# Kernel tuning notes

Hardware: AMD Instinct MI355X
Metric: run time of the kernel (lower is better)

## Reference

```python
import jax, jax.numpy as jnp
import numpy as np

N_AB, N_AG, F = 20000, 20000, 256
E_AB, E_AG, E_D = 320000, 320000, 640000
EPS = 1e-5


def _bn(x, gamma, beta):
    # BatchNorm1d, training-mode batch statistics (deterministic), biased variance
    mu = x.mean(0)
    var = x.var(0)
    return (x - mu) * jax.lax.rsqrt(var + EPS) * gamma + beta


def _gcn(x, ei, W, b, n):
    # PyG GCNConv: add self loops, symmetric deg^-1/2 normalization, scatter-add
    loop = jnp.arange(n, dtype=ei.dtype)
    src = jnp.concatenate([ei[0], loop])
    dst = jnp.concatenate([ei[1], loop])
    deg = jax.ops.segment_sum(jnp.ones_like(src, dtype=x.dtype), dst, num_segments=n)
    dinv = jax.lax.rsqrt(jnp.maximum(deg, 1.0))  # deg >= 1 due to self loops
    norm = dinv[src] * dinv[dst]                 # [E]
    h = x @ W                                    # [n, D]
    return jax.ops.segment_sum(h[src] * norm[:, None], dst, num_segments=n) + b


def _gat(x, ei, W, a_s, a_d, b, n, slope=0.2):
    # PyG GATConv, heads=1, add self loops; attention dropout off (eval mode)
    loop = jnp.arange(n, dtype=ei.dtype)
    src = jnp.concatenate([ei[0], loop])
    dst = jnp.concatenate([ei[1], loop])
    h = x @ W                                    # [n, D]
    e = jax.nn.leaky_relu((h @ a_s)[src] + (h @ a_d)[dst], slope)  # [E]
    # segment softmax over incoming edges of each dst node
    m = jax.ops.segment_max(e, dst, num_segments=n)
    ex = jnp.exp(e - m[dst])
    s = jax.ops.segment_sum(ex, dst, num_segments=n)
    alpha = ex / s[dst]
    return jax.ops.segment_sum(h[src] * alpha[:, None], dst, num_segments=n) + b


def setup_inputs() -> dict:
    key = jax.random.key(0)
    ks = jax.random.split(key, 20)
    sc = 1.0 / np.sqrt(F)
    sc2 = 1.0 / np.sqrt(2 * F)
    inp = {
        "x_ab": jax.random.normal(ks[0], (N_AB, F), jnp.float32),
        "x_ag": jax.random.normal(ks[1], (N_AG, F), jnp.float32),
        "W_gcn": jax.random.normal(ks[2], (F, F), jnp.float32) * sc,
        "b_gcn": jnp.zeros((F,), jnp.float32),
        "g1": jnp.ones((F,), jnp.float32),
        "be1": jnp.zeros((F,), jnp.float32),
        "W_aggcn": jax.random.normal(ks[3], (F, F), jnp.float32) * sc,
        "b_aggcn": jnp.zeros((F,), jnp.float32),
        "ag_g1": jnp.ones((F,), jnp.float32),
        "ag_be1": jnp.zeros((F,), jnp.float32),
        "W_gat": jax.random.normal(ks[4], (F, F), jnp.float32) * sc,
        "a_src": jax.random.normal(ks[5], (F,), jnp.float32) * sc,
        "a_dst": jax.random.normal(ks[6], (F,), jnp.float32) * sc,
        "b_gat": jnp.zeros((F,), jnp.float32),
        "W_gat2": jax.random.normal(ks[7], (F, F), jnp.float32) * sc,
        "a_src2": jax.random.normal(ks[8], (F,), jnp.float32) * sc,
        "a_dst2": jax.random.normal(ks[9], (F,), jnp.float32) * sc,
        "b_gat2": jnp.zeros((F,), jnp.float32),
        "ag_g2": jnp.ones((2 * F,), jnp.float32),
        "ag_be2": jnp.zeros((2 * F,), jnp.float32),
        "W_agfc": jax.random.normal(ks[10], (2 * F, 1), jnp.float32) * sc2,
        "b_agfc": jnp.zeros((1,), jnp.float32),
        "g2": jnp.ones((2 * F,), jnp.float32),
        "be2": jnp.zeros((2 * F,), jnp.float32),
        "W_fc": jax.random.normal(ks[11], (2 * F, 1), jnp.float32) * sc2,
        "b_fc": jnp.zeros((1,), jnp.float32),
        "edge_x_ab": jax.random.randint(ks[12], (2, E_AB), 0, N_AB, jnp.int32),
        "edge_x_ag": jax.random.randint(ks[13], (2, E_AG), 0, N_AG, jnp.int32),
        "edge_index_d": jax.random.randint(ks[14], (2, E_D), 0, N_AB + N_AG, jnp.int32),
    }
    return inp


def reference(x_ab, x_ag, W_gcn, b_gcn, g1, be1, W_aggcn, b_aggcn, ag_g1, ag_be1,
              W_gat, a_src, a_dst, b_gat, W_gat2, a_src2, a_dst2, b_gat2,
              ag_g2, ag_be2, W_agfc, b_agfc, g2, be2, W_fc, b_fc,
              edge_x_ab, edge_x_ag, edge_index_d):
    relu = jax.nn.relu
    h_ab = relu(_bn(_gcn(x_ab, edge_x_ab, W_gcn, b_gcn, N_AB), g1, be1))
    h_ag = relu(_bn(_gcn(x_ag, edge_x_ag, W_aggcn, b_aggcn, N_AG), ag_g1, ag_be1))
    # dropout layers are identity in eval mode
    n = N_AB + N_AG
    x = jnp.concatenate([h_ab, h_ag], axis=0)
    x = relu(_gat(x, edge_index_d, W_gat, a_src, a_dst, b_gat, n))
    x = _gat(x, edge_index_d, W_gat2, a_src2, a_dst2, b_gat2, n)
    x1, x2 = x[:N_AB], x[N_AB:]
    out_ag = relu(_bn(jnp.concatenate([x2, h_ag], axis=1), ag_g2, ag_be2)) @ W_agfc + b_agfc
    out_ab = relu(_bn(jnp.concatenate([x1, h_ab], axis=1), g2, be2)) @ W_fc + b_fc
    return out_ab, out_ag
```

## Files before the change

kernel.cpp:

```cpp
#include <hip/hip_runtime.h>
#include <hip/hip_bf16.h>
#include <stdint.h>

#define NF 256
#define EPSV 1e-5f
#define PB 160
#define MAXBUK 160

typedef unsigned short u16;
typedef unsigned int u32;
typedef short short8 __attribute__((ext_vector_type(8)));
typedef float floatx4 __attribute__((ext_vector_type(4)));

#define P_BGCN 0
#define P_G1 256
#define P_BE1 512
#define P_BAGG 768
#define P_AGG1 1024
#define P_AGBE1 1280
#define P_ASRC 1536
#define P_ADST 1792
#define P_BGAT 2048
#define P_ASRC2 2304
#define P_ADST2 2560
#define P_BGAT2 2816
#define P_G2 3072
#define P_BE2 3584
#define P_WFC 4096
#define P_AGG2 4608
#define P_AGBE2 5120
#define P_WAGFC 5632
#define P_BFC 6144
#define P_BAGFC 6145

__device__ __forceinline__ float bf2f(u16 u) {
    union { unsigned int i; float f; } v; v.i = ((unsigned int)u) << 16; return v.f;
}
__device__ __forceinline__ u16 f2bf(float f) {
    unsigned int x = __float_as_uint(f);
    unsigned int r = x + 0x7fffu + ((x >> 16) & 1u);
    return (u16)(r >> 16);
}
__device__ __forceinline__ float sane(float f) {
    return (f == f && fabsf(f) < 1e30f) ? f : 0.f;
}
__device__ __forceinline__ unsigned int zap2(unsigned int w) {
    if ((w & 0x00007F80u) == 0x00007F80u) w &= 0xFFFF0000u;
    if ((w & 0x7F800000u) == 0x7F800000u) w &= 0x0000FFFFu;
    return w;
}
__device__ __forceinline__ float lrelu(float x) { return x > 0.f ? x : 0.2f * x; }

__device__ __forceinline__ float4 ld4h(const u16* p) {
    uint2 u = *(const uint2*)p;
    float4 r;
    r.x = bf2f((u16)(u.x & 0xFFFFu)); r.y = bf2f((u16)(u.x >> 16));
    r.z = bf2f((u16)(u.y & 0xFFFFu)); r.w = bf2f((u16)(u.y >> 16));
    return r;
}
__device__ __forceinline__ void st4h(u16* p, float4 v) {
    uint2 u;
    u.x = (unsigned)f2bf(v.x) | ((unsigned)f2bf(v.y) << 16);
    u.y = (unsigned)f2bf(v.z) | ((unsigned)f2bf(v.w) << 16);
    *(uint2*)p = u;
}

__device__ __forceinline__ void fma8(const uint4 u, float a, float* acc) {
    acc[0] = fmaf(__uint_as_float(u.x << 16), a, acc[0]);
    acc[1] = fmaf(__uint_as_float(u.x & 0xFFFF0000u), a, acc[1]);
    acc[2] = fmaf(__uint_as_float(u.y << 16), a, acc[2]);
    acc[3] = fmaf(__uint_as_float(u.y & 0xFFFF0000u), a, acc[3]);
    acc[4] = fmaf(__uint_as_float(u.z << 16), a, acc[4]);
    acc[5] = fmaf(__uint_as_float(u.z & 0xFFFF0000u), a, acc[5]);
    acc[6] = fmaf(__uint_as_float(u.w << 16), a, acc[6]);
    acc[7] = fmaf(__uint_as_float(u.w & 0xFFFF0000u), a, acc[7]);
}
__device__ __forceinline__ void st8h(u16* p, const float* v) {
    uint4 u;
    u.x = (u32)f2bf(v[0]) | ((u32)f2bf(v[1]) << 16);
    u.y = (u32)f2bf(v[2]) | ((u32)f2bf(v[3]) << 16);
    u.z = (u32)f2bf(v[4]) | ((u32)f2bf(v[5]) << 16);
    u.w = (u32)f2bf(v[6]) | ((u32)f2bf(v[7]) << 16);
    *(uint4*)p = u;
}

__device__ __forceinline__ float wredsum(float v) {
#pragma unroll
    for (int o = 32; o > 0; o >>= 1) v += __shfl_xor(v, o, 64);
    return v;
}
__device__ __forceinline__ int wscan_incl(int x, int lane) {
#pragma unroll
    for (int o = 1; o < 64; o <<= 1) {
        int t = __shfl_up(x, o, 64);
        if (lane >= o) x += t;
    }
    return x;
}

__global__ void detect_k(const u16* __restrict__ x, int* __restrict__ flag) {
    __shared__ int cnt;
    if (threadIdx.x == 0) cnt = 0;
    __syncthreads();
    int c = 0;
#pragma unroll
    for (int k = 0; k < 4; ++k) {
        unsigned int u = x[2 * (threadIdx.x + 256 * k)];
        int e = (int)((u >> 7) & 0xFFu);
        if (u == 0u || (e >= 100 && e <= 140)) c++;
    }
    atomicAdd(&cnt, c);
    __syncthreads();
    if (threadIdx.x == 0) flag[0] = (cnt >= 512) ? 1 : 0;
}

__global__ void prep_k(const void* w0, const void* w1, const void* w2, const void* w3,
                       const void* p0, const void* p1, const void* p2, const void* p3,
                       const void* p4, const void* p5, const void* p6, const void* p7,
                       const void* p8, const void* p9, const void* p10, const void* p11,
                       const void* p12, const void* p13, const void* p14, const void* p15,
                       const void* p16, const void* p17, const void* p18, const void* p19,
                       u16* __restrict__ wtf, float* __restrict__ prm,
                       int* __restrict__ zb, int nz,
                       const int* __restrict__ flagp) {
    int f = flagp[0];
    int idx = blockIdx.x * 256 + threadIdx.x;
    if (idx < nz) zb[idx] = 0;
    if (idx < 262144) {
        const void* ws[4] = {w0, w1, w2, w3};
        int wi = idx >> 16;
        int rest = idx & 65535;
        int j = rest & 7;
        int lr = (rest >> 3) & 15;
        int q = (rest >> 7) & 3;
        int nf = (rest >> 9) & 15;
        int ks = (rest >> 13) & 7;
        int n = nf * 16 + lr;
        int k = ks * 32 + q * 8 + j;
        const void* W = ws[wi];
        u16 v;
        if (f) {
            v = ((const u16*)W)[k * NF + n];
            if ((v & 0x7F80u) == 0x7F80u) v = 0;
        } else {
            v = f2bf(sane(((const float*)W)[k * NF + n]));
        }
        wtf[idx] = v;
        return;
    }
    int pidx = idx - 262144;
    if (pidx >= 6146) return;
    const void* ptrs[20] = {p0, p1, p2, p3, p4, p5, p6, p7, p8, p9,
                            p10, p11, p12, p13, p14, p15, p16, p17, p18, p19};
    int t, j;
    if (pidx < 3072) { t = pidx >> 8; j = pidx & 255; }
    else if (pidx < 6144) { t = 12 + ((pidx - 3072) >> 9); j = (pidx - 3072) & 511; }
    else { t = 18 + (pidx - 6144); j = 0; }
    float v = f ? bf2f(((const u16*)ptrs[t])[j]) : ((const float*)ptrs[t])[j];
    prm[pidx] = sane(v);
}

__global__ __launch_bounds__(256) void bucket_cnt3_k(const int* e0, const int* e1,
                                                     const int* e2,
                                                     int* __restrict__ gbcnt) {
    int y = blockIdx.y;
    const int* ei = (y == 0) ? e0 : (y == 1) ? e1 : e2;
    int E = (y == 2) ? 640000 : 320000;
    int n = (y == 2) ? 40000 : 20000;
    int nbuk = (n + 255) >> 8;
    int base = blockIdx.x * 4096;
    if (base >= E) return;
    __shared__ int l[MAXBUK];
    if (threadIdx.x < nbuk) l[threadIdx.x] = 0;
    __syncthreads();
#pragma unroll
    for (int t = 0; t < 16; ++t) {
        int e = base + t * 256 + threadIdx.x;
        if (e < E) atomicAdd(&l[ei[E + e] >> 8], 1);
    }
    __syncthreads();
    if (threadIdx.x < nbuk) {
        int c = l[threadIdx.x];
        if (c) atomicAdd(&gbcnt[y * MAXBUK + threadIdx.x], c);
    }
}
__global__ __launch_bounds__(256) void bucket_scan3_k(const int* __restrict__ gbcnt,
                                                      int* __restrict__ bb,
                                                      int* rp0, int* rp1, int* rp2) {
    __shared__ int wp[4];
    int y = blockIdx.y;
    int n = (y == 2) ? 40000 : 20000;
    int E = (y == 2) ? 640000 : 320000;
    int nbuk = (n + 255) >> 8;
    int* rp = (y == 0) ? rp0 : (y == 1) ? rp1 : rp2;
    int lane = threadIdx.x & 63, wave = threadIdx.x >> 6;
    int v = (threadIdx.x < nbuk) ? gbcnt[y * MAXBUK + threadIdx.x] : 0;
    int x = wscan_incl(v, lane);
    if (lane == 63) wp[wave] = x;
    __syncthreads();
    int off = 0;
#pragma unroll
    for (int w = 0; w < 4; ++w) off += (w < wave) ? wp[w] : 0;
    if (threadIdx.x < nbuk) bb[y * (MAXBUK + 1) + threadIdx.x] = off + x - v;
    if (threadIdx.x == 0) {
        bb[y * (MAXBUK + 1) + nbuk] = E;
        rp[n] = E;
    }
}
__global__ __launch_bounds__(256) void bin3_k(const int* e0, const int* e1, const int* e2,
                                              const int* __restrict__ bb,
                                              int* __restrict__ gcur,
                                              u32* s0, u32* s1, u32* s2) {
    int y = blockIdx.y;
    const int* ei = (y == 0) ? e0 : (y == 1) ? e1 : e2;
    u32* stg = (y == 0) ? s0 : (y == 1) ? s1 : s2;
    int E = (y == 2) ? 640000 : 320000;
    int n = (y == 2) ? 40000 : 20000;
    int nbuk = (n + 255) >> 8;
    int base = blockIdx.x * 4096;
    if (base >= E) return;
    __shared__ int lcnt[MAXBUK];
    __shared__ int lbase[MAXBUK];
    if (threadIdx.x < nbuk) lcnt[threadIdx.x] = 0;
    __syncthreads();
#pragma unroll
    for (int t = 0; t < 16; ++t) {
        int e = base + t * 256 + threadIdx.x;
        if (e < E) atomicAdd(&lcnt[ei[E + e] >> 8], 1);
    }
    __syncthreads();
    if (threadIdx.x < nbuk) {
        int cnt = lcnt[threadIdx.x];
        int g = cnt ? atomicAdd(&gcur[y * MAXBUK + threadIdx.x], cnt) : 0;
        lbase[threadIdx.x] = bb[y * (MAXBUK + 1) + threadIdx.x] + g;
        lcnt[threadIdx.x] = 0;
    }
    __syncthreads();
#pragma unroll
    for (int t = 0; t < 16; ++t) {
        int e = base + t * 256 + threadIdx.x;
        if (e < E) {
            int s = ei[e], d = ei[E + e];
            int b = d >> 8;
            int r = atomicAdd(&lcnt[b], 1);
            stg[lbase[b] + r] = (u32)s | ((u32)(d & 255) << 16);
        }
    }
}
__global__ __launch_bounds__(256) void place3_k(const u32* s0, const u32* s1, const u32* s2,
                                                const int* __restrict__ bb,
                                                int* rp0, int* rp1, int* rp2,
                                                float* dv0, float* dv1,
                                                int* c0, int* c1, int* c2) {
    __shared__ int wp[4];
    __shared__ int lcnt[256];
    __shared__ int lrp[256];
    int y = blockIdx.y;
    int b = blockIdx.x;
    int n = (y == 2) ? 40000 : 20000;
    int nbuk = (n + 255) >> 8;
    if (b >= nbuk) return;
    const u32* stg = (y == 0) ? s0 : (y == 1) ? s1 : s2;
    int* rp = (y == 0) ? rp0 : (y == 1) ? rp1 : rp2;
    int* col = (y == 0) ? c0 : (y == 1) ? c1 : c2;
    int d0 = b << 8;
    int dn = min(256, n - d0);
    int base = bb[y * (MAXBUK + 1) + b];
    int endv = bb[y * (MAXBUK + 1) + b + 1];
    lcnt[threadIdx.x] = 0;
    __syncthreads();
    for (int j = base + threadIdx.x; j < endv; j += 256)
        atomicAdd(&lcnt[stg[j] >> 16], 1);
    __syncthreads();
    int lane = threadIdx.x & 63, wave = threadIdx.x >> 6;
    int v = lcnt[threadIdx.x];
    int x = wscan_incl(v, lane);
    if (lane == 63) wp[wave] = x;
    __syncthreads();
    int off = 0;
#pragma unroll
    for (int w = 0; w < 4; ++w) off += (w < wave) ? wp[w] : 0;
    int excl = base + off + x - v;
    lrp[threadIdx.x] = excl;
    if (threadIdx.x < dn) {
        rp[d0 + threadIdx.x] = excl;
        if (y == 0) dv0[d0 + threadIdx.x] = rsqrtf((float)(v + 1));
        else if (y == 1) dv1[d0 + threadIdx.x] = rsqrtf((float)(v + 1));
    }
    lcnt[threadIdx.x] = 0;
    __syncthreads();
    for (int j = base + threadIdx.x; j < endv; j += 256) {
        u32 rec = stg[j];
        int dl = (int)(rec >> 16);
        int s = (int)(rec & 0xFFFFu);
        int r = atomicAdd(&lcnt[dl], 1);
        col[lrp[dl] + r] = s;
    }
}

__global__ __launch_bounds__(256) void gemm2_k(const void* A0, const void* A1,
                                               const u16* __restrict__ Wtf0,
                                               const u16* __restrict__ Wtf1,
                                               const int* __restrict__ flagp,
                                               u16* __restrict__ C, int M) {
    int f = flagp[0];
    int y = blockIdx.y;
    const void* Aptr = y ? A1 : A0;
    const u16* Wtf = y ? Wtf1 : Wtf0;
    u16* Cp = C + (size_t)y * M * NF;
    int wave = threadIdx.x >> 6, lane = threadIdx.x & 63;
    int lr = lane & 15, q = lane >> 4;
    int arow = blockIdx.x * 64 + wave * 16 + lr;
    bool rok = arow < M;
    floatx4 acc[16];
#pragma unroll
    for (int nf = 0; nf < 16; ++nf) acc[nf] = (floatx4){0.f, 0.f, 0.f, 0.f};
    const u16* a16 = (const u16*)Aptr + (size_t)arow * NF;
    const float* a32 = (const float*)Aptr + (size_t)arow * NF;
#pragma unroll
    for (int ks = 0; ks < 8; ++ks) {
        int kk = ks * 32 + q * 8;
        union { u16 s[8]; uint4 u; short8 v; } a;
        if (!rok) {
            a.u = make_uint4(0u, 0u, 0u, 0u);
        } else if (f) {
            a.u = *(const uint4*)(a16 + kk);
            a.u.x = zap2(a.u.x); a.u.y = zap2(a.u.y);
            a.u.z = zap2(a.u.z); a.u.w = zap2(a.u.w);
        } else {
            float4 f0 = *(const float4*)(a32 + kk);
            float4 f1 = *(const float4*)(a32 + kk + 4);
            a.s[0] = f2bf(sane(f0.x)); a.s[1] = f2bf(sane(f0.y));
            a.s[2] = f2bf(sane(f0.z)); a.s[3] = f2bf(sane(f0.w));
            a.s[4] = f2bf(sane(f1.x)); a.s[5] = f2bf(sane(f1.y));
            a.s[6] = f2bf(sane(f1.z)); a.s[7] = f2bf(sane(f1.w));
        }
        const u16* bbase = Wtf + ks * 8192 + lane * 8;
#pragma unroll
        for (int nf = 0; nf < 16; ++nf) {
            short8 b = *(const short8*)(bbase + nf * 512);
            acc[nf] = __builtin_amdgcn_mfma_f32_16x16x32_bf16(a.v, b, acc[nf], 0, 0, 0);
        }
    }
#pragma unroll
    for (int nf = 0; nf < 16; ++nf) {
#pragma unroll
        for (int rr = 0; rr < 4; ++rr) {
            int gr = blockIdx.x * 64 + wave * 16 + q * 4 + rr;
            if (gr < M) Cp[(size_t)gr * NF + nf * 16 + lr] = f2bf(acc[nf][rr]);
        }
    }
}

__global__ __launch_bounds__(256) void gemm_gat_k(const u16* __restrict__ Aptr,
                                                  const u16* __restrict__ Wtf,
                                                  u16* __restrict__ C, int M,
                                                  const float* __restrict__ as_,
                                                  const float* __restrict__ ad_,
                                                  float* __restrict__ es,
                                                  float* __restrict__ ed) {
    int wave = threadIdx.x >> 6, lane = threadIdx.x & 63;
    int lr = lane & 15, q = lane >> 4;
    int arow = blockIdx.x * 64 + wave * 16 + lr;
    bool rok = arow < M;
    floatx4 acc[16];
#pragma unroll
    for (int nf = 0; nf < 16; ++nf) acc[nf] = (floatx4){0.f, 0.f, 0.f, 0.f};
    const u16* a16 = Aptr + (size_t)arow * NF;
#pragma unroll
    for (int ks = 0; ks < 8; ++ks) {
        int kk = ks * 32 + q * 8;
        union { uint4 u; short8 v; } a;
        a.u = rok ? *(const uint4*)(a16 + kk) : make_uint4(0u, 0u, 0u, 0u);
        const u16* bbase = Wtf + ks * 8192 + lane * 8;
#pragma unroll
        for (int nf = 0; nf < 16; ++nf) {
            short8 b = *(const short8*)(bbase + nf * 512);
            acc[nf] = __builtin_amdgcn_mfma_f32_16x16x32_bf16(a.v, b, acc[nf], 0, 0, 0);
        }
    }
#pragma unroll
    for (int nf = 0; nf < 16; ++nf) {
#pragma unroll
        for (int rr = 0; rr < 4; ++rr) {
            int gr = blockIdx.x * 64 + wave * 16 + q * 4 + rr;
            if (gr < M) C[(size_t)gr * NF + nf * 16 + lr] = f2bf(acc[nf][rr]);
        }
    }
    float asl[16], adl[16];
#pragma unroll
    for (int nf = 0; nf < 16; ++nf) { asl[nf] = as_[nf * 16 + lr]; adl[nf] = ad_[nf * 16 + lr]; }
#pragma unroll
    for (int rr = 0; rr < 4; ++rr) {
        float s1 = 0.f, s2 = 0.f;
#pragma unroll
        for (int nf = 0; nf < 16; ++nf) {
            s1 += acc[nf][rr] * asl[nf];
            s2 += acc[nf][rr] * adl[nf];
        }
#pragma unroll
        for (int o = 1; o < 16; o <<= 1) {
            s1 += __shfl_xor(s1, o, 64);
            s2 += __shfl_xor(s2, o, 64);
        }
        int gr = blockIdx.x * 64 + wave * 16 + q * 4 + rr;
        if (lr == 0 && gr < M) { es[gr] = s1; ed[gr] = s2; }
    }
}

__global__ __launch_bounds__(256) void gcn_csr2_k(const u16* __restrict__ h,
                                                  const int* rp0, const int* rp1,
                                                  const int* c0, const int* c1,
                                                  const float* dv0, const float* dv1,
                                                  const float* __restrict__ prm,
                                                  u16* __restrict__ out, int n) {
    int y = blockIdx.y;
    const int* rp = y ? rp1 : rp0;
    const int* col = y ? c1 : c0;
    const float* dinv = y ? dv1 : dv0;
    const float* b = prm + (y ? P_BAGG : P_BGCN);
    const u16* hb = h + (size_t)y * n * NF;
    u16* ob = out + (size_t)y * n * NF;
    int wave = threadIdx.x >> 6, lane = threadIdx.x & 63;
    int half = lane >> 5, sl = lane & 31;
    int i = blockIdx.x * 4 + wave;
    if (i >= n) return;
    int c = sl * 8;
    int beg = rp[i], end = rp[i + 1];
    float di = dinv[i];
    float acc[8] = {0.f, 0.f, 0.f, 0.f, 0.f, 0.f, 0.f, 0.f};
    float selfw = half ? 0.f : di * di;
    uint4 uv = *(const uint4*)(hb + (size_t)i * NF + c);
    fma8(uv, selfw, acc);
    int j = beg + half;
    for (; j + 2 < end; j += 4) {
        int s0 = col[j], s1 = col[j + 2];
        float n0 = dinv[s0] * di, n1 = dinv[s1] * di;
        uint4 u0 = *(const uint4*)(hb + (size_t)s0 * NF + c);
        uint4 u1 = *(const uint4*)(hb + (size_t)s1 * NF + c);
        fma8(u0, n0, acc);
        fma8(u1, n1, acc);
    }
    for (; j < end; j += 2) {
        int s = col[j];
        float nr = dinv[s] * di;
        uint4 u = *(const uint4*)(hb + (size_t)s * NF + c);
        fma8(u, nr, acc);
    }
#pragma unroll
    for (int k = 0; k < 8; ++k) acc[k] += __shfl_xor(acc[k], 32, 64);
#pragma unroll
    for (int k = 0; k < 8; ++k) acc[k] += b[c + k];
    if (half == 0) st8h(ob + (size_t)i * NF + c, acc);
}

__global__ void bn_stats2_k(const u16* __restrict__ x, int n,
                            float* __restrict__ psum, float* __restrict__ psq) {
    int y = blockIdx.y;
    int c = threadIdx.x;
    int r0 = blockIdx.x * 128;
    int rend = min(r0 + 128, n);
    const u16* xb = x + (size_t)y * n * NF;
    float s = 0.f, qq = 0.f;
    for (int r = r0; r < rend; ++r) {
        float v = bf2f(xb[(size_t)r * NF + c]);
        s += v; qq += v * v;
    }
    size_t o = (size_t)(y * PB + blockIdx.x) * 512 + c;
    psum[o] = s; psq[o] = qq;
}
__global__ void bn_fin2_k(const float* __restrict__ psum, const float* __restrict__ psq,
                          float* __restrict__ stg, int n, int nb) {
    int y = blockIdx.y;
    int c = threadIdx.x;
    float s = 0.f, qq = 0.f;
    for (int b = 0; b < nb; ++b) {
        size_t o = (size_t)(y * PB + b) * 512 + c;
        s += psum[o]; qq += psq[o];
    }
    float inv_n = 1.0f / (float)n;
    float mean = s * inv_n;
    float var = fmaxf(qq * inv_n - mean * mean, 0.f);
    stg[y * 512 + c] = mean;
    stg[y * 512 + 256 + c] = rsqrtf(var + EPSV);
}
__global__ void bn_apply2_k(const u16* __restrict__ x, const float* __restrict__ stg,
                            const float* __restrict__ prm, u16* __restrict__ out, int n) {
    int y = blockIdx.y;
    int t = blockIdx.x * 256 + threadIdx.x;
    if (t >= n * (NF / 8)) return;
    int c = (t & 31) * 8;
    const float* st = stg + y * 512;
    const float* g = prm + (y ? P_AGG1 : P_G1);
    const float* be = prm + (y ? P_AGBE1 : P_BE1);
    uint4 u = *(const uint4*)(x + (size_t)y * n * NF + (size_t)t * 8);
    float v[8];
    v[0] = __uint_as_float(u.x << 16); v[1] = __uint_as_float(u.x & 0xFFFF0000u);
    v[2] = __uint_as_float(u.y << 16); v[3] = __uint_as_float(u.y & 0xFFFF0000u);
    v[4] = __uint_as_float(u.z << 16); v[5] = __uint_as_float(u.z & 0xFFFF0000u);
    v[6] = __uint_as_float(u.w << 16); v[7] = __uint_as_float(u.w & 0xFFFF0000u);
    float r[8];
#pragma unroll
    for (int k = 0; k < 8; ++k) {
        int cc = c + k;
        float w = (v[k] - st[cc]) * st[256 + cc] * g[cc] + be[cc];
        r[k] = fmaxf(w, 0.f);
    }
    st8h(out + (size_t)y * n * NF + (size_t)t * 8, r);
}

__global__ __launch_bounds__(256) void gat_csr_k(const u16* __restrict__ h,
                                                 const int* __restrict__ rp,
                                                 const int* __restrict__ col,
                                                 const float* __restrict__ es,
                                                 const float* __restrict__ ed,
                                                 const float* __restrict__ b,
                                                 u16* __restrict__ out, int n,
                                                 int do_relu) {
    int wave = threadIdx.x >> 6, lane = threadIdx.x & 63;
    int half = lane >> 5, sl = lane & 31;
    int i = blockIdx.x * 4 + wave;
    if (i >= n) return;
    int beg = rp[i], end = rp[i + 1];
    float edi = ed[i];
    int c = sl * 8;
    float acc[8] = {0.f, 0.f, 0.f, 0.f, 0.f, 0.f, 0.f, 0.f};
    float ws = __expf(lrelu(es[i] + edi));
    float selfw = half ? 0.f : ws;
    float ssum = selfw;
    uint4 uv = *(const uint4*)(h + (size_t)i * NF + c);
    fma8(uv, selfw, acc);
    int j = beg + half;
    for (; j + 2 < end; j += 4) {
        int s0 = col[j], s1 = col[j + 2];
        float a0 = __expf(lrelu(es[s0] + edi));
        float a1 = __expf(lrelu(es[s1] + edi));
        uint4 u0 = *(const uint4*)(h + (size_t)s0 * NF + c);
        uint4 u1 = *(const uint4*)(h + (size_t)s1 * NF + c);
        ssum += a0 + a1;
        fma8(u0, a0, acc);
        fma8(u1, a1, acc);
    }
    for (; j < end; j += 2) {
        int s = col[j];
        float a = __expf(lrelu(es[s] + edi));
        uint4 u = *(const uint4*)(h + (size_t)s * NF + c);
        ssum += a;
        fma8(u, a, acc);
    }
    ssum += __shfl_xor(ssum, 32, 64);
#pragma unroll
    for (int k = 0; k < 8; ++k) acc[k] += __shfl_xor(acc[k], 32, 64);
    float inv = 1.0f / ssum;
#pragma unroll
    for (int k = 0; k < 8; ++k) {
        acc[k] = b[c + k] + acc[k] * inv;
        if (do_relu) acc[k] = fmaxf(acc[k], 0.f);
    }
    if (half == 0) st8h(out + (size_t)i * NF + c, acc);
}

__global__ void bn_stats_cat2_k(const u16* __restrict__ xp, const u16* __restrict__ hp,
                                int n, float* __restrict__ psum, float* __restrict__ psq) {
    int y = blockIdx.y;
    int c = threadIdx.x;
    int r0 = blockIdx.x * 128;
    int rend = min(r0 + 128, n);
    const u16* src = ((c < 256) ? xp : hp) + (size_t)y * n * NF;
    int cc = c & 255;
    float s = 0.f, qq = 0.f;
    for (int r = r0; r < rend; ++r) {
        float v = bf2f(src[(size_t)r * NF + cc]);
        s += v; qq += v * v;
    }
    size_t o = (size_t)(y * PB + blockIdx.x) * 512 + c;
    psum[o] = s; psq[o] = qq;
}
__global__ void bn_fin_cat2_k(const float* __restrict__ psum, const float* __restrict__ psq,
                              float* __restrict__ stc, int n, int nb) {
    int y = blockIdx.y;
    int c = threadIdx.x;
    float s = 0.f, qq = 0.f;
    for (int b = 0; b < nb; ++b) {
        size_t o = (size_t)(y * PB + b) * 512 + c;
        s += psum[o]; qq += psq[o];
    }
    float inv_n = 1.0f / (float)n;
    float mean = s * inv_n;
    float var = fmaxf(qq * inv_n - mean * mean, 0.f);
    stc[y * 1024 + c] = mean;
    stc[y * 1024 + 512 + c] = rsqrtf(var + EPSV);
}
__global__ void final2_k(const u16* __restrict__ xp, const u16* __restrict__ hp,
                         const float* __restrict__ stc, const float* __restrict__ prm,
                         float* __restrict__ out, int n) {
    int y = blockIdx.y;
    int wave = threadIdx.x >> 6, lane = threadIdx.x & 63;
    int i = blockIdx.x * 4 + wave;
    if (i >= n) return;
    const float* st = stc + y * 1024;
    const float* g = prm + (y ? P_AGG2 : P_G2);
    const float* be = prm + (y ? P_AGBE2 : P_BE2);
    const float* w = prm + (y ? P_WAGFC : P_WFC);
    float bias = prm[y ? P_BAGFC : P_BFC];
    const u16* src = (((lane < 32) ? xp : hp) + (size_t)y * n * NF) + (size_t)i * NF
                     + (lane < 32 ? lane * 8 : (lane - 32) * 8);
    uint4 u = *(const uint4*)src;
    float vv[8];
    vv[0] = bf2f((u16)(u.x & 0xFFFFu)); vv[1] = bf2f((u16)(u.x >> 16));
    vv[2] = bf2f((u16)(u.y & 0xFFFFu)); vv[3] = bf2f((u16)(u.y >> 16));
    vv[4] = bf2f((u16)(u.z & 0xFFFFu)); vv[5] = bf2f((u16)(u.z >> 16));
    vv[6] = bf2f((u16)(u.w & 0xFFFFu)); vv[7] = bf2f((u16)(u.w >> 16));
    int c0 = lane * 8;
    float acc = 0.f;
#pragma unroll
    for (int j = 0; j < 8; ++j) {
        int c = c0 + j;
        float v = (vv[j] - st[c]) * st[512 + c] * g[c] + be[c];
        v = fmaxf(v, 0.f);
        acc += v * w[c];
    }
    acc = wredsum(acc);
    if (lane == 0) out[(size_t)y * 20000 + i] = acc + bias;
}

extern "C" void kernel_launch(void* const* d_in, const int* in_sizes, int n_in,
                              void* d_out, int out_size, void* d_ws, size_t ws_size,
                              hipStream_t stream) {
    const void* x_ab = d_in[0];
    const void* x_ag = d_in[1];
    const int* e_ab = (const int*)d_in[26];
    const int* e_ag = (const int*)d_in[27];
    const int* e_d = (const int*)d_in[28];

    const int NAB = 20000, NT = 40000;
    const int EAB = 320000, EAG = 320000, ED = 640000;

    u16* hcat = (u16*)d_ws;
    u16* bufA = hcat + (size_t)NT * NF;
    u16* bufB = bufA + (size_t)NT * NF;
    u16* wt4 = bufB + (size_t)NT * NF;
    float* dv0 = (float*)(wt4 + 4 * 65536);
    float* dv1 = dv0 + NAB;
    float* es = dv1 + NAB;
    float* edv = es + NT;
    float* stg2 = edv + NT;
    float* stc = stg2 + 1024;
    float* psum = stc + 2048;
    float* psq = psum + 2 * PB * 512;
    float* prm = psq + 2 * PB * 512;
    int* flag = (int*)(prm + 8192);
    int* rp_ab = flag + 16;
    int* rp_ag = rp_ab + NAB + 1;
    int* rp_d = rp_ag + NAB + 1;
    int* gbcnt = rp_d + NT + 1;
    int* gcur = gbcnt + 3 * MAXBUK;
    int* bb = gcur + 3 * MAXBUK;
    int* col_ab = bb + 3 * (MAXBUK + 1);
    int* col_ag = col_ab + EAB;
    int* col_d = col_ag + EAG;
    u32* stg_ab = (u32*)(col_d + ED);
    u32* stg_ag = stg_ab + EAB;
    u32* stg_d = stg_ag + EAG;

    u16* wt_gcn = wt4;
    u16* wt_aggcn = wt4 + 65536;
    u16* wt_gat = wt4 + 2 * 65536;
    u16* wt_gat2 = wt4 + 3 * 65536;

    dim3 t256(256), t512(512);
    const int nbg = (NAB + 127) / 128;

    detect_k<<<dim3(1), t256, 0, stream>>>((const u16*)x_ab, flag);
    prep_k<<<dim3(1049), t256, 0, stream>>>(
        d_in[2], d_in[6], d_in[10], d_in[14],
        d_in[3], d_in[4], d_in[5], d_in[7], d_in[8], d_in[9],
        d_in[11], d_in[12], d_in[13], d_in[15], d_in[16], d_in[17],
        d_in[22], d_in[23], d_in[24], d_in[18], d_in[19], d_in[20],
        d_in[25], d_in[21], wt4, prm, gbcnt, 6 * MAXBUK + 3 * (MAXBUK + 1), flag);

    bucket_cnt3_k<<<dim3(157, 3), t256, 0, stream>>>(e_ab, e_ag, e_d, gbcnt);
    bucket_scan3_k<<<dim3(1, 3), t256, 0, stream>>>(gbcnt, bb, rp_ab, rp_ag, rp_d);
    bin3_k<<<dim3(157, 3), t256, 0, stream>>>(e_ab, e_ag, e_d, bb, gcur,
                                              stg_ab, stg_ag, stg_d);
    place3_k<<<dim3(157, 3), t256, 0, stream>>>(stg_ab, stg_ag, stg_d, bb,
                                                rp_ab, rp_ag, rp_d, dv0, dv1,
                                                col_ab, col_ag, col_d);

    gemm2_k<<<dim3((NAB + 63) / 64, 2), t256, 0, stream>>>(x_ab, x_ag, wt_gcn, wt_aggcn,
                                                           flag, bufA, NAB);
    gcn_csr2_k<<<dim3((NAB + 3) / 4, 2), t256, 0, stream>>>(bufA, rp_ab, rp_ag,
                                                            col_ab, col_ag, dv0, dv1,
                                                            prm, bufB, NAB);
    bn_stats2_k<<<dim3(nbg, 2), t256, 0, stream>>>(bufB, NAB, psum, psq);
    bn_fin2_k<<<dim3(1, 2), t256, 0, stream>>>(psum, psq, stg2, NAB, nbg);
    bn_apply2_k<<<dim3((NAB * NF / 8 + 255) / 256, 2), t256, 0, stream>>>(bufB, stg2, prm,
                                                                          hcat, NAB);

    gemm_gat_k<<<dim3((NT + 63) / 64), t256, 0, stream>>>(hcat, wt_gat, bufA, NT,
                                                          prm + P_ASRC, prm + P_ADST,
                                                          es, edv);
    gat_csr_k<<<dim3((NT + 3) / 4), t256, 0, stream>>>(bufA, rp_d, col_d, es, edv,
                                                       prm + P_BGAT, bufB, NT, 1);
    gemm_gat_k<<<dim3((NT + 63) / 64), t256, 0, stream>>>(bufB, wt_gat2, bufA, NT,
                                                          prm + P_ASRC2, prm + P_ADST2,
                                                          es, edv);
    gat_csr_k<<<dim3((NT + 3) / 4), t256, 0, stream>>>(bufA, rp_d, col_d, es, edv,
                                                       prm + P_BGAT2, bufB, NT, 0);

    bn_stats_cat2_k<<<dim3(nbg, 2), t512, 0, stream>>>(bufB, hcat, NAB, psum, psq);
    bn_fin_cat2_k<<<dim3(1, 2), t512, 0, stream>>>(psum, psq, stc, NAB, nbg);
    final2_k<<<dim3((NAB + 3) / 4, 2), t256, 0, stream>>>(bufB, hcat, stc, prm,
                                                          (float*)d_out, NAB);
}
```

Measured before the change: 599.7 us.

## Split CSR gather kernels into 32-column feature slices across blocks

The GCN and GAT aggregation kernels now assign each block one of 8 column slices of 32 features for 32 nodes. Each node is handled by 8 threads loading 8-byte chunks, where before a whole wave covered a node with 16-byte loads split across two half-waves. The aim is to keep the gathered working set per block smaller and more L2-friendly, and to drop the cross-half shuffle reduction. In exchange, col/dinv/es lookups and exp computations are repeated 8 times per edge across slices, loads are narrower, and divergence within a wave grows because 8 nodes of different degree now share one wave.

After: 693.4 us. 15.6% more time.

```diff
diff --git a/kernel.cpp b/kernel.cpp
--- a/kernel.cpp
+++ b/kernel.cpp
@@ -64,16 +64,17 @@
     u.y = (unsigned)f2bf(v.z) | ((unsigned)f2bf(v.w) << 16);
     *(uint2*)p = u;
 }
-
-__device__ __forceinline__ void fma8(const uint4 u, float a, float* acc) {
+__device__ __forceinline__ void fma4u(const uint2 u, float a, float* acc) {
     acc[0] = fmaf(__uint_as_float(u.x << 16), a, acc[0]);
     acc[1] = fmaf(__uint_as_float(u.x & 0xFFFF0000u), a, acc[1]);
     acc[2] = fmaf(__uint_as_float(u.y << 16), a, acc[2]);
     acc[3] = fmaf(__uint_as_float(u.y & 0xFFFF0000u), a, acc[3]);
-    acc[4] = fmaf(__uint_as_float(u.z << 16), a, acc[4]);
-    acc[5] = fmaf(__uint_as_float(u.z & 0xFFFF0000u), a, acc[5]);
-    acc[6] = fmaf(__uint_as_float(u.w << 16), a, acc[6]);
-    acc[7] = fmaf(__uint_as_float(u.w & 0xFFFF0000u), a, acc[7]);
+}
+__device__ __forceinline__ void st4hp(u16* p, const float* v) {
+    uint2 u;
+    u.x = (u32)f2bf(v[0]) | ((u32)f2bf(v[1]) << 16);
+    u.y = (u32)f2bf(v[2]) | ((u32)f2bf(v[3]) << 16);
+    *(uint2*)p = u;
 }
 __device__ __forceinline__ void st8h(u16* p, const float* v) {
     uint4 u;
@@ -421,37 +422,35 @@
     const float* b = prm + (y ? P_BAGG : P_BGCN);
     const u16* hb = h + (size_t)y * n * NF;
     u16* ob = out + (size_t)y * n * NF;
-    int wave = threadIdx.x >> 6, lane = threadIdx.x & 63;
-    int half = lane >> 5, sl = lane & 31;
-    int i = blockIdx.x * 4 + wave;
+    int bid = blockIdx.x;
+    int g = bid & 7, chunk = bid >> 3;
+    int i = chunk * 32 + (threadIdx.x >> 3);
     if (i >= n) return;
-    int c = sl * 8;
+    int c = g * 32 + (threadIdx.x & 7) * 4;
     int beg = rp[i], end = rp[i + 1];
     float di = dinv[i];
-    float acc[8] = {0.f, 0.f, 0.f, 0.f, 0.f, 0.f, 0.f, 0.f};
-    float selfw = half ? 0.f : di * di;
-    uint4 uv = *(const uint4*)(hb + (size_t)i * NF + c);
-    fma8(uv, selfw, acc);
-    int j = beg + half;
-    for (; j + 2 < end; j += 4) {
-        int s0 = col[j], s1 = col[j + 2];
+    float acc[4] = {0.f, 0.f, 0.f, 0.f};
+    uint2 uv = *(const uint2*)(hb + (size_t)i * NF + c);
+    fma4u(uv, di * di, acc);
+    int j = beg;
+    for (; j + 1 < end; j += 2) {
+        int s0 = col[j], s1 = col[j + 1];
         float n0 = dinv[s0] * di, n1 = dinv[s1] * di;
-        uint4 u0 = *(const uint4*)(hb + (size_t)s0 * NF + c);
-        uint4 u1 = *(const uint4*)(hb + (size_t)s1 * NF + c);
-        fma8(u0, n0, acc);
-        fma8(u1, n1, acc);
-    }
-    for (; j < end; j += 2) {
+        uint2 u0 = *(const uint2*)(hb + (size_t)s0 * NF + c);
+        uint2 u1 = *(const uint2*)(hb + (size_t)s1 * NF + c);
+        fma4u(u0, n0, acc);
+        fma4u(u1, n1, acc);
+    }
+    if (j < end) {
         int s = col[j];
         float nr = dinv[s] * di;
-        uint4 u = *(const uint4*)(hb + (size_t)s * NF + c);
-        fma8(u, nr, acc);
-    }
-#pragma unroll
-    for (int k = 0; k < 8; ++k) acc[k] += __shfl_xor(acc[k], 32, 64);
-#pragma unroll
-    for (int k = 0; k < 8; ++k) acc[k] += b[c + k];
-    if (half == 0) st8h(ob + (size_t)i * NF + c, acc);
+        uint2 u = *(const uint2*)(hb + (size_t)s * NF + c);
+        fma4u(u, nr, acc);
+    }
+    float r[4];
+#pragma unroll
+    for (int k = 0; k < 4; ++k) r[k] = acc[k] + b[c + k];
+    st4hp(ob + (size_t)i * NF + c, r);
 }
 
 __global__ void bn_stats2_k(const u16* __restrict__ x, int n,
@@ -517,47 +516,44 @@
                                                  const float* __restrict__ b,
                                                  u16* __restrict__ out, int n,
                                                  int do_relu) {
-    int wave = threadIdx.x >> 6, lane = threadIdx.x & 63;
-    int half = lane >> 5, sl = lane & 31;
-    int i = blockIdx.x * 4 + wave;
+    int bid = blockIdx.x;
+    int g = bid & 7, chunk = bid >> 3;
+    int i = chunk * 32 + (threadIdx.x >> 3);
     if (i >= n) return;
+    int c = g * 32 + (threadIdx.x & 7) * 4;
     int beg = rp[i], end = rp[i + 1];
     float edi = ed[i];
-    int c = sl * 8;
-    float acc[8] = {0.f, 0.f, 0.f, 0.f, 0.f, 0.f, 0.f, 0.f};
     float ws = __expf(lrelu(es[i] + edi));
-    float selfw = half ? 0.f : ws;
-    float ssum = selfw;
-    uint4 uv = *(const uint4*)(h + (size_t)i * NF + c);
-    fma8(uv, selfw, acc);
-    int j = beg + half;
-    for (; j + 2 < end; j += 4) {
-        int s0 = col[j], s1 = col[j + 2];
+    float ssum = ws;
+    float acc[4] = {0.f, 0.f, 0.f, 0.f};
+    uint2 uv = *(const uint2*)(h + (size_t)i * NF + c);
+    fma4u(uv, ws, acc);
+    int j = beg;
+    for (; j + 1 < end; j += 2) {
+        int s0 = col[j], s1 = col[j + 1];
         float a0 = __expf(lrelu(es[s0] + edi));
         float a1 = __expf(lrelu(es[s1] + edi));
-        uint4 u0 = *(const uint4*)(h + (size_t)s0 * NF + c);
-        uint4 u1 = *(const uint4*)(h + (size_t)s1 * NF + c);
+        uint2 u0 = *(const uint2*)(h + (size_t)s0 * NF + c);
+        uint2 u1 = *(const uint2*)(h + (size_t)s1 * NF + c);
         ssum += a0 + a1;
-        fma8(u0, a0, acc);
-        fma8(u1, a1, acc);
-    }
-    for (; j < end; j += 2) {
+        fma4u(u0, a0, acc);
+        fma4u(u1, a1, acc);
+    }
+    if (j < end) {
         int s = col[j];
         float a = __expf(lrelu(es[s] + edi));
-        uint4 u = *(const uint4*)(h + (size_t)s * NF + c);
+        uint2 u = *(const uint2*)(h + (size_t)s * NF + c);
         ssum += a;
-        fma8(u, a, acc);
-    }
-    ssum += __shfl_xor(ssum, 32, 64);
-#pragma unroll
-    for (int k = 0; k < 8; ++k) acc[k] += __shfl_xor(acc[k], 32, 64);
+        fma4u(u, a, acc);
+    }
     float inv = 1.0f / ssum;
-#pragma unroll
-    for (int k = 0; k < 8; ++k) {
-        acc[k] = b[c + k] + acc[k] * inv;
-        if (do_relu) acc[k] = fmaxf(acc[k], 0.f);
-    }
-    if (half == 0) st8h(out + (size_t)i * NF + c, acc);
+    float r[4];
+#pragma unroll
+    for (int k = 0; k < 4; ++k) {
+        r[k] = b[c + k] + acc[k] * inv;
+        if (do_relu) r[k] = fmaxf(r[k], 0.f);
+    }
+    st4hp(out + (size_t)i * NF + c, r);
 }
 
 __global__ void bn_stats_cat2_k(const u16* __restrict__ xp, const u16* __restrict__ hp,
@@ -689,9 +685,9 @@
 
     gemm2_k<<<dim3((NAB + 63) / 64, 2), t256, 0, stream>>>(x_ab, x_ag, wt_gcn, wt_aggcn,
                                                            flag, bufA, NAB);
-    gcn_csr2_k<<<dim3((NAB + 3) / 4, 2), t256, 0, stream>>>(bufA, rp_ab, rp_ag,
-                                                            col_ab, col_ag, dv0, dv1,
-                                                            prm, bufB, NAB);
+    gcn_csr2_k<<<dim3(8 * ((NAB + 31) / 32), 2), t256, 0, stream>>>(bufA, rp_ab, rp_ag,
+                                                                    col_ab, col_ag, dv0, dv1,
+                                                                    prm, bufB, NAB);
     bn_stats2_k<<<dim3(nbg, 2), t256, 0, stream>>>(bufB, NAB, psum, psq);
     bn_fin2_k<<<dim3(1, 2), t256, 0, stream>>>(psum, psq, stg2, NAB, nbg);
     bn_apply2_k<<<dim3((NAB * NF / 8 + 255) / 256, 2), t256, 0, stream>>>(bufB, stg2, prm,
@@ -700,13 +696,13 @@
     gemm_gat_k<<<dim3((NT + 63) / 64), t256, 0, stream>>>(hcat, wt_gat, bufA, NT,
                                                           prm + P_ASRC, prm + P_ADST,
                                                           es, edv);
-    gat_csr_k<<<dim3((NT + 3) / 4), t256, 0, stream>>>(bufA, rp_d, col_d, es, edv,
-                                                       prm + P_BGAT, bufB, NT, 1);
+    gat_csr_k<<<dim3(8 * ((NT + 31) / 32)), t256, 0, stream>>>(bufA, rp_d, col_d, es, edv,
+                                                               prm + P_BGAT, bufB, NT, 1);
     gemm_gat_k<<<dim3((NT + 63) / 64), t256, 0, stream>>>(bufB, wt_gat2, bufA, NT,
                                                           prm + P_ASRC2, prm + P_ADST2,
                                                           es, edv);
-    gat_csr_k<<<dim3((NT + 3) / 4), t256, 0, stream>>>(bufA, rp_d, col_d, es, edv,
-                                                       prm + P_BGAT2, bufB, NT, 0);
+    gat_csr_k<<<dim3(8 * ((NT + 31) / 32)), t256, 0, stream>>>(bufA, rp_d, col_d, es, edv,
+                                                               prm + P_BGAT2, bufB, NT, 0);
 
     bn_stats_cat2_k<<<dim3(nbg, 2), t512, 0, stream>>>(bufB, hcat, NAB, psum, psq);
     bn_fin_cat2_k<<<dim3(1, 2), t512, 0, stream>>>(psum, psq, stc, NAB, nbg);
```
